# Optimization experiments

Hardware: AMD Instinct MI355X
Metric: run time of the kernel (lower is better)

## Reference

```python
import jax, jax.numpy as jnp
import numpy as np

N = 100000
E = 1600000
IN, HID, OUT = 128, 256, 47


def _glorot(key, shape):
    fan_in, fan_out = shape
    lim = np.sqrt(6.0 / (fan_in + fan_out))
    return jax.random.uniform(key, shape, jnp.float32, -lim, lim)


def setup_inputs() -> dict:
    key = jax.random.key(0)
    ks = jax.random.split(key, 12)
    x = jax.random.normal(ks[0], (N, IN), jnp.float32)
    src = jax.random.randint(ks[1], (E,), 0, N, jnp.int32)
    dst = jax.random.randint(ks[2], (E,), 0, N, jnp.int32)
    dims = [(IN, HID), (HID, HID), (HID, OUT)]
    inp = {"x": x, "src": src, "dst": dst}
    for i, (di, do) in enumerate(dims, 1):
        inp[f"w_self{i}"] = _glorot(ks[2 + 3 * i - 2], (di, do))
        inp[f"w_neigh{i}"] = _glorot(ks[2 + 3 * i - 1], (di, do))
        inp[f"b{i}"] = jnp.zeros((do,), jnp.float32)
    return inp


def sage_conv(x, src, dst, w_self, w_neigh, b):
    n = x.shape[0]
    msg = x[src]                                              # [E, d] gather
    summed = jax.ops.segment_sum(msg, dst, num_segments=n)    # [N, d]
    deg = jax.ops.segment_sum(jnp.ones((src.shape[0],), x.dtype), dst, num_segments=n)
    h_neigh = summed / jnp.maximum(deg, 1.0)[:, None]         # mean aggregate
    return x @ w_self + h_neigh @ w_neigh + b


def reference(x, src, dst, w_self1, w_neigh1, b1, w_self2, w_neigh2, b2, w_self3, w_neigh3, b3):
    h = sage_conv(x, src, dst, w_self1, w_neigh1, b1)
    h = jax.nn.relu(h)  # dropout = identity in eval mode
    h = sage_conv(h, src, dst, w_self2, w_neigh2, b2)
    h = jax.nn.relu(h)
    h = sage_conv(h, src, dst, w_self3, w_neigh3, b3)
    return h
```

## Files before the change

kernel.cpp:

```cpp
#include <hip/hip_runtime.h>

#define N_NODES 100000
#define N_EDGES 1600000

typedef __attribute__((ext_vector_type(8))) _Float16 half8;
typedef __attribute__((ext_vector_type(4))) _Float16 half4v;
typedef __attribute__((ext_vector_type(4))) float floatx4;


__global__ void deg_rank(const int* __restrict__ dst, int* __restrict__ deg,
                         int* __restrict__ rank, int e) {
    int i = blockIdx.x * blockDim.x + threadIdx.x;
    if (i < e) rank[i] = atomicAdd(&deg[dst[i]], 1);
}

__global__ __launch_bounds__(256) void scan_partial(const int* __restrict__ deg,
                                                    int* __restrict__ bsum, int n) {
    __shared__ int wsum[4];
    int t = threadIdx.x;
    int base = blockIdx.x * 2048 + t * 8;
    int tsum = 0;
    #pragma unroll
    for (int k = 0; k < 8; ++k) {
        int idx = base + k;
        tsum += (idx < n) ? deg[idx] : 0;
    }
    #pragma unroll
    for (int d = 1; d < 64; d <<= 1) tsum += __shfl_xor(tsum, d, 64);
    if ((t & 63) == 0) wsum[t >> 6] = tsum;
    __syncthreads();
    if (t == 0) bsum[blockIdx.x] = wsum[0] + wsum[1] + wsum[2] + wsum[3];
}

__global__ void scan_blocksums(const int* __restrict__ bsum, int* __restrict__ bbase, int nb) {
    int t = threadIdx.x;
    int v = (t < nb) ? bsum[t] : 0;
    int s = v;
    #pragma unroll
    for (int d = 1; d < 64; d <<= 1) {
        int u = __shfl_up(s, d, 64);
        if (t >= d) s += u;
    }
    if (t < nb) bbase[t] = s - v;
    if (t == 63) bbase[nb] = s;
}

__global__ __launch_bounds__(256) void scan_write(const int* __restrict__ deg,
                                                  const int* __restrict__ bbase,
                                                  int* __restrict__ offs, int n, int nb) {
    __shared__ int wsum[4];
    int t = threadIdx.x;
    int lane = t & 63, w = t >> 6;
    int base = blockIdx.x * 2048 + t * 8;
    int v[8];
    #pragma unroll
    for (int k = 0; k < 8; ++k) {
        int idx = base + k;
        v[k] = (idx < n) ? deg[idx] : 0;
    }
    int tsum = 0;
    #pragma unroll
    for (int k = 0; k < 8; ++k) { int x = v[k]; v[k] = tsum; tsum += x; }
    int s = tsum;
    #pragma unroll
    for (int d = 1; d < 64; d <<= 1) {
        int u = __shfl_up(s, d, 64);
        if (lane >= d) s += u;
    }
    if (lane == 63) wsum[w] = s;
    __syncthreads();
    int wb = 0;
    for (int j = 0; j < w; ++j) wb += wsum[j];
    int texcl = bbase[blockIdx.x] + wb + (s - tsum);
    #pragma unroll
    for (int k = 0; k < 8; ++k) {
        int idx = base + k;
        if (idx < n) offs[idx] = texcl + v[k];
    }
    if (blockIdx.x == 0 && t == 0) offs[n] = bbase[nb];
}

__global__ void fill_csr2(const int* __restrict__ src, const int* __restrict__ dst,
                          const int* __restrict__ offs, const int* __restrict__ rank,
                          int* __restrict__ csr, int e) {
    int i = blockIdx.x * blockDim.x + threadIdx.x;
    if (i < e) csr[offs[dst[i]] + rank[i]] = src[i];
}


__global__ void cvt_f16(const float4* __restrict__ in, half4v* __restrict__ oh, int n4) {
    int i = blockIdx.x * blockDim.x + threadIdx.x;
    if (i >= n4) return;
    float4 v = in[i];
    half4v h;
    h[0] = (_Float16)v.x; h[1] = (_Float16)v.y;
    h[2] = (_Float16)v.z; h[3] = (_Float16)v.w;
    oh[i] = h;
}


__global__ void prep_all(const float* __restrict__ ws1, const float* __restrict__ wn1,
                         const float* __restrict__ ws2, const float* __restrict__ wn2,
                         const float* __restrict__ ws3, const float* __restrict__ wn3,
                         _Float16* __restrict__ o1s, _Float16* __restrict__ o1n,
                         _Float16* __restrict__ o2s, _Float16* __restrict__ o2n,
                         _Float16* __restrict__ o3c) {
    int i = blockIdx.x * blockDim.x + threadIdx.x;
    if (i < 65536) {
        const float* W = (i < 32768) ? ws1 : wn1;
        _Float16* O = (i < 32768) ? o1s : o1n;
        int j = i & 32767;
        int nn = j >> 7, k = j & 127;
        O[j] = (_Float16)W[k * 256 + nn];
    } else if (i < 196608) {
        int j = i - 65536;
        const float* W = (j < 65536) ? ws2 : wn2;
        _Float16* O = (j < 65536) ? o2s : o2n;
        j &= 65535;
        int nn = j >> 8, k = j & 255;
        O[j] = (_Float16)W[k * 256 + nn];
    } else if (i < 221184) {
        int j = i - 196608;
        const float* W = (j < 12288) ? ws3 : wn3;
        _Float16* O = o3c + ((j < 12288) ? 0 : 12288);
        j = (j < 12288) ? j : j - 12288;
        int nn = j >> 8, k = j & 255;
        O[j] = (nn < 47) ? (_Float16)W[k * 47 + nn] : (_Float16)0.f;
    }
}


__global__ __launch_bounds__(256) void aggP(const _Float16* __restrict__ Xp,
                                            const int* __restrict__ csr,
                                            const int* __restrict__ offs,
                                            _Float16* __restrict__ Pp, int n) {
    int node = blockIdx.x * 4 + (threadIdx.x >> 6);
    int lane = threadIdx.x & 63;
    int qtr = lane >> 4;
    int sl = lane & 15;
    if (node >= n) return;
    int e0 = offs[node], e1 = offs[node + 1];
    float a[8] = {0.f, 0.f, 0.f, 0.f, 0.f, 0.f, 0.f, 0.f};
    int e = e0;
    for (; e + 16 <= e1; e += 16) {
        int s0 = csr[e + qtr];
        int s1 = csr[e + 4 + qtr];
        int s2 = csr[e + 8 + qtr];
        int s3 = csr[e + 12 + qtr];
        half8 u0 = ((const half8*)(Xp + (size_t)s0 * 128))[sl];
        half8 u1 = ((const half8*)(Xp + (size_t)s1 * 128))[sl];
        half8 u2 = ((const half8*)(Xp + (size_t)s2 * 128))[sl];
        half8 u3 = ((const half8*)(Xp + (size_t)s3 * 128))[sl];
        #pragma unroll
        for (int j = 0; j < 8; ++j) a[j] += (float)u0[j];
        #pragma unroll
        for (int j = 0; j < 8; ++j) a[j] += (float)u1[j];
        #pragma unroll
        for (int j = 0; j < 8; ++j) a[j] += (float)u2[j];
        #pragma unroll
        for (int j = 0; j < 8; ++j) a[j] += (float)u3[j];
    }
    for (; e + 8 <= e1; e += 8) {
        int s0 = csr[e + qtr];
        int s1 = csr[e + 4 + qtr];
        half8 u0 = ((const half8*)(Xp + (size_t)s0 * 128))[sl];
        half8 u1 = ((const half8*)(Xp + (size_t)s1 * 128))[sl];
        #pragma unroll
        for (int j = 0; j < 8; ++j) a[j] += (float)u0[j];
        #pragma unroll
        for (int j = 0; j < 8; ++j) a[j] += (float)u1[j];
    }
    for (; e + 4 <= e1; e += 4) {
        int s = csr[e + qtr];
        half8 u = ((const half8*)(Xp + (size_t)s * 128))[sl];
        #pragma unroll
        for (int j = 0; j < 8; ++j) a[j] += (float)u[j];
    }
    int rem = e1 - e;
    if (qtr < rem) {
        int s = csr[e + qtr];
        half8 u = ((const half8*)(Xp + (size_t)s * 128))[sl];
        #pragma unroll
        for (int j = 0; j < 8; ++j) a[j] += (float)u[j];
    }
    #pragma unroll
    for (int j = 0; j < 8; ++j) {
        a[j] += __shfl_xor(a[j], 16);
        a[j] += __shfl_xor(a[j], 32);
    }
    if (lane < 16) {
        float inv = 1.0f / fmaxf((float)(e1 - e0), 1.0f);
        half8 rh;
        #pragma unroll
        for (int j = 0; j < 8; ++j) rh[j] = (_Float16)(a[j] * inv);
        ((half8*)(Pp + (size_t)node * 128))[sl] = rh;
    }
}

__global__ __launch_bounds__(256) void agg_l3(const _Float16* __restrict__ Y,
                                              const float* __restrict__ S,
                                              const int* __restrict__ csr,
                                              const int* __restrict__ offs,
                                              float* __restrict__ out, int n) {
    int node = blockIdx.x * 4 + (threadIdx.x >> 6);
    int lane = threadIdx.x & 63;
    int qtr = lane >> 4;
    int sl = lane & 15;
    int c = sl < 12 ? sl : 11;
    if (node >= n) return;
    int e0 = offs[node], e1 = offs[node + 1];
    float a0 = 0.f, a1 = 0.f, a2 = 0.f, a3 = 0.f;
    int e = e0;
    for (; e + 8 <= e1; e += 8) {
        int s0 = csr[e + qtr];
        int s1 = csr[e + 4 + qtr];
        half4v f0 = ((const half4v*)(Y + (size_t)s0 * 48))[c];
        half4v f1 = ((const half4v*)(Y + (size_t)s1 * 48))[c];
        a0 += (float)f0[0] + (float)f1[0];
        a1 += (float)f0[1] + (float)f1[1];
        a2 += (float)f0[2] + (float)f1[2];
        a3 += (float)f0[3] + (float)f1[3];
    }
    for (; e + 4 <= e1; e += 4) {
        int s = csr[e + qtr];
        half4v f = ((const half4v*)(Y + (size_t)s * 48))[c];
        a0 += (float)f[0]; a1 += (float)f[1]; a2 += (float)f[2]; a3 += (float)f[3];
    }
    int rem = e1 - e;
    if (qtr < rem) {
        int s = csr[e + qtr];
        half4v f = ((const half4v*)(Y + (size_t)s * 48))[c];
        a0 += (float)f[0]; a1 += (float)f[1]; a2 += (float)f[2]; a3 += (float)f[3];
    }
    a0 += __shfl_xor(a0, 16); a0 += __shfl_xor(a0, 32);
    a1 += __shfl_xor(a1, 16); a1 += __shfl_xor(a1, 32);
    a2 += __shfl_xor(a2, 16); a2 += __shfl_xor(a2, 32);
    a3 += __shfl_xor(a3, 16); a3 += __shfl_xor(a3, 32);
    if (lane < 12) {
        float inv = 1.0f / fmaxf((float)(e1 - e0), 1.0f);
        float4 sv = ((const float4*)(S + (size_t)node * 48))[c];
        float r[4] = {sv.x + a0 * inv, sv.y + a1 * inv, sv.z + a2 * inv, sv.w + a3 * inv};
        #pragma unroll
        for (int k = 0; k < 4; ++k) {
            int col = c * 4 + k;
            if (col < 47) out[(size_t)node * 47 + col] = r[k];
        }
    }
}


template <int NTILES, int OUTFMT, int SPP, int PHASES>
__global__ __launch_bounds__(256, 3) void gemm64r(
    const _Float16* __restrict__ A1h, const _Float16* __restrict__ A2h,
    const _Float16* __restrict__ W1, const _Float16* __restrict__ W2,
    const float* __restrict__ bias, float* __restrict__ outS, _Float16* __restrict__ outY,
    _Float16* __restrict__ outh, int n, int relu) {
    constexpr int NPAD = NTILES * 16;
    constexpr int LDT = 36;
    constexpr int NSTEPS = SPP * PHASES;
    constexpr int K = SPP * 32;
    __shared__ _Float16 Bs[2][NPAD * LDT];

    const int t = threadIdx.x;
    const int bm = blockIdx.x * 64;
    const int colbase = blockIdx.y * NPAD;
    const int lane = t & 63;
    const int w = t >> 6;
    const int quad = lane >> 4;
    const int tl = lane & 15;
    const int r0 = bm + w * 16 + tl;
    const size_t PS = (size_t)n * 128;

    floatx4 acc[NTILES];
    #pragma unroll
    for (int j = 0; j < NTILES; ++j) acc[j] = (floatx4){0.f, 0.f, 0.f, 0.f};

    half8 areg[NSTEPS];
    #pragma unroll
    for (int ph = 0; ph < PHASES; ++ph) {
        const _Float16* Ah = (ph == 0) ? A1h : A2h;
        #pragma unroll
        for (int st = 0; st < SPP; ++st) {
            int kq = st * 32 + quad * 8;
            const _Float16* Ab = Ah + ((kq >> 7) ? PS : (size_t)0) + (kq & 127);
            half8 d = (half8){0};
            if (r0 < n) d = *(const half8*)(Ab + (size_t)r0 * 128);
            areg[ph * SPP + st] = d;
        }
    }

    half8 pb0, pb1, pb2, pb3;
    auto wload = [&](int s2) {
        int ph2 = (s2 >= SPP) ? 1 : 0;
        int k02 = (ph2 ? s2 - SPP : s2) * 32;
        const _Float16* W = ph2 ? W2 : W1;
        const half8* p = (const half8*)(W + (size_t)(colbase + t) * K + k02);
        pb0 = p[0]; pb1 = p[1]; pb2 = p[2]; pb3 = p[3];
    };

    if (t < NPAD) {
        wload(0);
        *(half8*)&Bs[0][t * LDT + 0]  = pb0;
        *(half8*)&Bs[0][t * LDT + 8]  = pb1;
        *(half8*)&Bs[0][t * LDT + 16] = pb2;
        *(half8*)&Bs[0][t * LDT + 24] = pb3;
        if (NSTEPS > 1) wload(1);
    }
    __syncthreads();

    #pragma unroll
    for (int s = 0; s < NSTEPS; ++s) {
        const int cur = s & 1;
        if (s + 1 < NSTEPS && t < NPAD) {
            *(half8*)&Bs[cur ^ 1][t * LDT + 0]  = pb0;
            *(half8*)&Bs[cur ^ 1][t * LDT + 8]  = pb1;
            *(half8*)&Bs[cur ^ 1][t * LDT + 16] = pb2;
            *(half8*)&Bs[cur ^ 1][t * LDT + 24] = pb3;
            if (s + 2 < NSTEPS) wload(s + 2);
        }
        half8 ca = areg[s];
        #pragma unroll
        for (int nt = 0; nt < NTILES; ++nt) {
            half8 bh = *(const half8*)&Bs[cur][(nt * 16 + tl) * LDT + quad * 8];
            acc[nt] = __builtin_amdgcn_mfma_f32_16x16x32_f16(ca, bh, acc[nt], 0, 0, 0);
        }
        asm volatile("s_waitcnt lgkmcnt(0)" ::: "memory");
        __builtin_amdgcn_sched_barrier(0);
        __builtin_amdgcn_s_barrier();
    }

    #pragma unroll
    for (int nt = 0; nt < NTILES; ++nt) {
        int gc = colbase + nt * 16 + tl;
        #pragma unroll
        for (int r = 0; r < 4; ++r) {
            int gr = bm + w * 16 + quad * 4 + r;
            if (gr >= n) continue;
            float v = acc[nt][r];
            if (OUTFMT == 1) {
                v += bias[gc];
                if (relu) v = fmaxf(v, 0.f);
                outh[(size_t)(gc >> 7) * PS + (size_t)gr * 128 + (gc & 127)] = (_Float16)v;
            } else {
                if (gc < 48) {
                    v += (gc < 47) ? bias[gc] : 0.f;
                    outS[(size_t)gr * 48 + gc] = v;
                } else {
                    outY[(size_t)gr * 48 + (gc - 48)] = (_Float16)v;
                }
            }
        }
    }
}


template <int NTILES, int OUTFMT>
__global__ __launch_bounds__(256, 2) void gemm_mfma(
    const _Float16* __restrict__ A1h, const _Float16* __restrict__ A2h,
    const _Float16* __restrict__ W1, const _Float16* __restrict__ W2,
    const float* __restrict__ bias, float* __restrict__ outS, _Float16* __restrict__ outY,
    _Float16* __restrict__ outh, int n, int K, int dout, int relu, int phases) {
    constexpr int NPAD = NTILES * 16;
    constexpr int LDT = 36;
    __shared__ _Float16 Bs[2][NPAD * LDT];

    const int t = threadIdx.x;
    const int bm = blockIdx.x * 128;
    const int lane = t & 63;
    const int w = t >> 6;
    const int quad = lane >> 4;
    const int tl = lane & 15;
    const int r0 = bm + w * 32 + tl;
    const int r1 = r0 + 16;
    const size_t PS = (size_t)n * 128;

    floatx4 acc[2][NTILES];
    #pragma unroll
    for (int i = 0; i < 2; ++i)
        #pragma unroll
        for (int j = 0; j < NTILES; ++j) acc[i][j] = (floatx4){0.f, 0.f, 0.f, 0.f};

    const int spp = K >> 5;
    const int nsteps = phases * spp;

    half8 pb0, pb1, pb2, pb3;
    half8 a0A = {0}, a1A = {0}, a0B = {0}, a1B = {0};

    auto wload = [&](int s2) {
        int ph2 = (s2 >= spp) ? 1 : 0;
        int k02 = (ph2 ? s2 - spp : s2) << 5;
        const _Float16* W = ph2 ? W2 : W1;
        const half8* p = (const half8*)(W + (size_t)t * K + k02);
        pb0 = p[0]; pb1 = p[1]; pb2 = p[2]; pb3 = p[3];
    };
    auto aload = [&](int s2, half8& d0, half8& d1) {
        int ph2 = (s2 >= spp) ? 1 : 0;
        int k02 = (ph2 ? s2 - spp : s2) << 5;
        const _Float16* Ah = ph2 ? A2h : A1h;
        int kq = k02 + quad * 8;
        const _Float16* Ab = Ah + ((kq >> 7) ? PS : (size_t)0) + (kq & 127);
        d0 = (half8){0}; d1 = (half8){0};
        if (r0 < n) d0 = *(const half8*)(Ab + (size_t)r0 * 128);
        if (r1 < n) d1 = *(const half8*)(Ab + (size_t)r1 * 128);
    };

    if (t < NPAD) {
        wload(0);
        *(half8*)&Bs[0][t * LDT + 0]  = pb0;
        *(half8*)&Bs[0][t * LDT + 8]  = pb1;
        *(half8*)&Bs[0][t * LDT + 16] = pb2;
        *(half8*)&Bs[0][t * LDT + 24] = pb3;
        wload(1);
    }
    aload(0, a0A, a1A);
    aload(1, a0B, a1B);
    __syncthreads();

    for (int s = 0; s < nsteps; s += 2) {
        {
            if (s + 1 < nsteps && t < NPAD) {
                *(half8*)&Bs[1][t * LDT + 0]  = pb0;
                *(half8*)&Bs[1][t * LDT + 8]  = pb1;
                *(half8*)&Bs[1][t * LDT + 16] = pb2;
                *(half8*)&Bs[1][t * LDT + 24] = pb3;
                if (s + 2 < nsteps) wload(s + 2);
            }
            half8 ca0 = a0A, ca1 = a1A;
            if (s + 2 < nsteps) aload(s + 2, a0A, a1A);
            #pragma unroll
            for (int nt = 0; nt < NTILES; ++nt) {
                half8 bh = *(const half8*)&Bs[0][(nt * 16 + tl) * LDT + quad * 8];
                acc[0][nt] = __builtin_amdgcn_mfma_f32_16x16x32_f16(ca0, bh, acc[0][nt], 0, 0, 0);
                acc[1][nt] = __builtin_amdgcn_mfma_f32_16x16x32_f16(ca1, bh, acc[1][nt], 0, 0, 0);
            }
            asm volatile("s_waitcnt lgkmcnt(0)" ::: "memory");
            __builtin_amdgcn_sched_barrier(0);
            __builtin_amdgcn_s_barrier();
        }
        {
            int s1 = s + 1;
            if (s1 + 1 < nsteps && t < NPAD) {
                *(half8*)&Bs[0][t * LDT + 0]  = pb0;
                *(half8*)&Bs[0][t * LDT + 8]  = pb1;
                *(half8*)&Bs[0][t * LDT + 16] = pb2;
                *(half8*)&Bs[0][t * LDT + 24] = pb3;
                if (s1 + 2 < nsteps) wload(s1 + 2);
            }
            half8 ca0 = a0B, ca1 = a1B;
            if (s1 + 2 < nsteps) aload(s1 + 2, a0B, a1B);
            #pragma unroll
            for (int nt = 0; nt < NTILES; ++nt) {
                half8 bh = *(const half8*)&Bs[1][(nt * 16 + tl) * LDT + quad * 8];
                acc[0][nt] = __builtin_amdgcn_mfma_f32_16x16x32_f16(ca0, bh, acc[0][nt], 0, 0, 0);
                acc[1][nt] = __builtin_amdgcn_mfma_f32_16x16x32_f16(ca1, bh, acc[1][nt], 0, 0, 0);
            }
            asm volatile("s_waitcnt lgkmcnt(0)" ::: "memory");
            __builtin_amdgcn_sched_barrier(0);
            __builtin_amdgcn_s_barrier();
        }
    }

    #pragma unroll
    for (int mt = 0; mt < 2; ++mt) {
        #pragma unroll
        for (int nt = 0; nt < NTILES; ++nt) {
            int gc = nt * 16 + tl;
            if (OUTFMT == 1 && gc >= dout) continue;
            #pragma unroll
            for (int r = 0; r < 4; ++r) {
                int gr = bm + w * 32 + mt * 16 + quad * 4 + r;
                if (gr >= n) continue;
                float v = acc[mt][nt][r];
                if (OUTFMT == 1) {
                    v += bias[gc];
                    if (relu) v = fmaxf(v, 0.f);
                    outh[(size_t)(gc >> 7) * PS + (size_t)gr * 128 + (gc & 127)] = (_Float16)v;
                } else {
                    if (gc < 48) {
                        v += (gc < 47) ? bias[gc] : 0.f;
                        outS[(size_t)gr * 48 + gc] = v;
                    } else {
                        outY[(size_t)gr * 48 + (gc - 48)] = (_Float16)v;
                    }
                }
            }
        }
    }
}

extern "C" void kernel_launch(void* const* d_in, const int* in_sizes, int n_in,
                              void* d_out, int out_size, void* d_ws, size_t ws_size,
                              hipStream_t stream) {
    (void)in_sizes; (void)n_in; (void)out_size;
    const int N = N_NODES, E = N_EDGES;
    const float* x = (const float*)d_in[0];
    const int* src = (const int*)d_in[1];
    const int* dst = (const int*)d_in[2];
    const float* w_self1 = (const float*)d_in[3];
    const float* w_neigh1 = (const float*)d_in[4];
    const float* b1 = (const float*)d_in[5];
    const float* w_self2 = (const float*)d_in[6];
    const float* w_neigh2 = (const float*)d_in[7];
    const float* b2 = (const float*)d_in[8];
    const float* w_self3 = (const float*)d_in[9];
    const float* w_neigh3 = (const float*)d_in[10];
    const float* b3 = (const float*)d_in[11];
    float* out = (float*)d_out;

    _Float16* Ph = (_Float16*)d_ws;
    _Float16* Hh = Ph + (size_t)N * 256;
    int* deg = (int*)(Hh + (size_t)N * 256);
    int* offs = deg + N;
    int* csr = offs + N + 4;
    _Float16* wbuf = (_Float16*)(csr + E);
    _Float16* w1s = wbuf;
    _Float16* w1n = w1s + 32768;
    _Float16* w2s = w1n + 32768;
    _Float16* w2n = w2s + 65536;
    _Float16* w3c = w2n + 65536;
    int* bsum = (int*)(w3c + 24576);
    int* bbase = bsum + 64;
    int* rank = (int*)Ph;
    _Float16* xh = Ph + (size_t)N * 128;
    float* S = (float*)Ph;
    _Float16* Y = (_Float16*)(S + (size_t)N * 48);
    size_t used = (size_t)((char*)(bbase + 64) - (char*)d_ws);
    used = (used + 255) & ~(size_t)255;
    _Float16* H2 = (_Float16*)((char*)d_ws + used);
    const bool dbuf = (used + (size_t)N * 256 * sizeof(_Float16)) <= ws_size;

    const int NB = (N + 2047) / 2048;

    hipMemsetAsync(deg, 0, N * sizeof(int), stream);
    deg_rank<<<(E + 255) / 256, 256, 0, stream>>>(dst, deg, rank, E);
    scan_partial<<<NB, 256, 0, stream>>>(deg, bsum, N);
    scan_blocksums<<<1, 64, 0, stream>>>(bsum, bbase, NB);
    scan_write<<<NB, 256, 0, stream>>>(deg, bbase, offs, N, NB);
    fill_csr2<<<(E + 255) / 256, 256, 0, stream>>>(src, dst, offs, rank, csr, E);

    cvt_f16<<<(N * 128 / 4 + 255) / 256, 256, 0, stream>>>((const float4*)x, (half4v*)xh,
                                                           N * 128 / 4);
    prep_all<<<(221184 + 255) / 256, 256, 0, stream>>>(w_self1, w_neigh1, w_self2, w_neigh2,
                                                       w_self3, w_neigh3, w1s, w1n, w2s, w2n,
                                                       w3c);

    const int g64 = (N + 63) / 64;
    int aggGrid = (N + 3) / 4;

    aggP<<<aggGrid, 256, 0, stream>>>(xh, csr, offs, Ph, N);
    gemm64r<8, 1, 4, 2><<<dim3(g64, 2), 256, 0, stream>>>(xh, Ph, w1s, w1n, b1, nullptr,
                                                          nullptr, Hh, N, 1);
    aggP<<<aggGrid, 256, 0, stream>>>(Hh, csr, offs, Ph, N);
    aggP<<<aggGrid, 256, 0, stream>>>(Hh + (size_t)N * 128, csr, offs, Ph + (size_t)N * 128, N);
    const _Float16* Hcur;
    if (dbuf) {
        gemm64r<8, 1, 8, 2><<<dim3(g64, 2), 256, 0, stream>>>(Hh, Ph, w2s, w2n, b2, nullptr,
                                                              nullptr, H2, N, 1);
        Hcur = H2;
    } else {
        gemm_mfma<16, 1><<<(N + 127) / 128, 256, 0, stream>>>(Hh, Ph, w2s, w2n, b2, nullptr,
                                                              nullptr, Hh, N, 256, 256, 1, 2);
        Hcur = Hh;
    }
    gemm64r<6, 2, 8, 1><<<dim3(g64, 1), 256, 0, stream>>>(Hcur, nullptr, w3c, nullptr, b3,
                                                          S, Y, nullptr, N, 0);
    agg_l3<<<aggGrid, 256, 0, stream>>>(Y, S, csr, offs, out, N);
}
```

Measured before the change: 636.4 us.

## Keep weight tiles in registers and loop over row tiles per block

Replaces the LDS double-buffered weight staging GEMM with a kernel where each wave holds its weight columns in registers for the whole K dimension and walks eight 16-row tiles, double-buffering A loads in registers. This removes LDS writes, barriers and repeated weight loads per 64-row block, and amortises the weight fetch over 128 rows. In exchange register pressure rises sharply (for layer 2 about 32 half8 B registers per lane), which may lower occupancy. Layer 3 now wastes a wave's worth of columns (96 of 128), clamped by ncols.

```diff
diff --git a/kernel.cpp b/kernel.cpp
--- a/kernel.cpp
+++ b/kernel.cpp
@@ -249,107 +249,100 @@
 }
 
 
-template <int NTILES, int OUTFMT, int SPP, int PHASES>
-__global__ __launch_bounds__(256, 3) void gemm64r(
+template <int NTPW, int OUTFMT, int SPP, int PHASES, int MT>
+__global__ __launch_bounds__(256) void gemm_breg(
     const _Float16* __restrict__ A1h, const _Float16* __restrict__ A2h,
     const _Float16* __restrict__ W1, const _Float16* __restrict__ W2,
-    const float* __restrict__ bias, float* __restrict__ outS, _Float16* __restrict__ outY,
-    _Float16* __restrict__ outh, int n, int relu) {
-    constexpr int NPAD = NTILES * 16;
-    constexpr int LDT = 36;
+    const float* __restrict__ bias, float* __restrict__ outS,
+    _Float16* __restrict__ outY, _Float16* __restrict__ outh,
+    int n, int relu, int ncols) {
     constexpr int NSTEPS = SPP * PHASES;
     constexpr int K = SPP * 32;
-    __shared__ _Float16 Bs[2][NPAD * LDT];
-
     const int t = threadIdx.x;
-    const int bm = blockIdx.x * 64;
-    const int colbase = blockIdx.y * NPAD;
     const int lane = t & 63;
     const int w = t >> 6;
     const int quad = lane >> 4;
     const int tl = lane & 15;
-    const int r0 = bm + w * 16 + tl;
+    const int colw = blockIdx.y * 128 + w * (NTPW * 16);
     const size_t PS = (size_t)n * 128;
 
-    floatx4 acc[NTILES];
-    #pragma unroll
-    for (int j = 0; j < NTILES; ++j) acc[j] = (floatx4){0.f, 0.f, 0.f, 0.f};
-
-    half8 areg[NSTEPS];
-    #pragma unroll
-    for (int ph = 0; ph < PHASES; ++ph) {
-        const _Float16* Ah = (ph == 0) ? A1h : A2h;
-        #pragma unroll
-        for (int st = 0; st < SPP; ++st) {
-            int kq = st * 32 + quad * 8;
-            const _Float16* Ab = Ah + ((kq >> 7) ? PS : (size_t)0) + (kq & 127);
-            half8 d = (half8){0};
-            if (r0 < n) d = *(const half8*)(Ab + (size_t)r0 * 128);
-            areg[ph * SPP + st] = d;
-        }
-    }
-
-    half8 pb0, pb1, pb2, pb3;
-    auto wload = [&](int s2) {
-        int ph2 = (s2 >= SPP) ? 1 : 0;
-        int k02 = (ph2 ? s2 - SPP : s2) * 32;
-        const _Float16* W = ph2 ? W2 : W1;
-        const half8* p = (const half8*)(W + (size_t)(colbase + t) * K + k02);
-        pb0 = p[0]; pb1 = p[1]; pb2 = p[2]; pb3 = p[3];
+    half8 breg[NTPW][NSTEPS];
+    #pragma unroll
+    for (int nt = 0; nt < NTPW; ++nt) {
+        int col = colw + nt * 16 + tl;
+        int colc = (col < ncols) ? col : (ncols - 1);
+        #pragma unroll
+        for (int ph = 0; ph < PHASES; ++ph) {
+            const _Float16* W = (ph == 0) ? W1 : W2;
+            const half8* p = (const half8*)(W + (size_t)colc * K + quad * 8);
+            #pragma unroll
+            for (int st = 0; st < SPP; ++st)
+                breg[nt][ph * SPP + st] = p[st * 4];
+        }
+    }
+
+    auto loadA = [&](int rowbase, half8 (&a)[NSTEPS]) {
+        int r0 = rowbase + tl;
+        #pragma unroll
+        for (int ph = 0; ph < PHASES; ++ph) {
+            const _Float16* Ah = (ph == 0) ? A1h : A2h;
+            #pragma unroll
+            for (int st = 0; st < SPP; ++st) {
+                int kq = st * 32 + quad * 8;
+                const _Float16* Ab = Ah + ((kq >> 7) ? PS : (size_t)0) + (kq & 127);
+                half8 d = (half8){0};
+                if (r0 < n) d = *(const half8*)(Ab + (size_t)r0 * 128);
+                a[ph * SPP + st] = d;
+            }
+        }
     };
 
-    if (t < NPAD) {
-        wload(0);
-        *(half8*)&Bs[0][t * LDT + 0]  = pb0;
-        *(half8*)&Bs[0][t * LDT + 8]  = pb1;
-        *(half8*)&Bs[0][t * LDT + 16] = pb2;
-        *(half8*)&Bs[0][t * LDT + 24] = pb3;
-        if (NSTEPS > 1) wload(1);
-    }
-    __syncthreads();
-
-    #pragma unroll
-    for (int s = 0; s < NSTEPS; ++s) {
-        const int cur = s & 1;
-        if (s + 1 < NSTEPS && t < NPAD) {
-            *(half8*)&Bs[cur ^ 1][t * LDT + 0]  = pb0;
-            *(half8*)&Bs[cur ^ 1][t * LDT + 8]  = pb1;
-            *(half8*)&Bs[cur ^ 1][t * LDT + 16] = pb2;
-            *(half8*)&Bs[cur ^ 1][t * LDT + 24] = pb3;
-            if (s + 2 < NSTEPS) wload(s + 2);
-        }
-        half8 ca = areg[s];
-        #pragma unroll
-        for (int nt = 0; nt < NTILES; ++nt) {
-            half8 bh = *(const half8*)&Bs[cur][(nt * 16 + tl) * LDT + quad * 8];
-            acc[nt] = __builtin_amdgcn_mfma_f32_16x16x32_f16(ca, bh, acc[nt], 0, 0, 0);
-        }
-        asm volatile("s_waitcnt lgkmcnt(0)" ::: "memory");
-        __builtin_amdgcn_sched_barrier(0);
-        __builtin_amdgcn_s_barrier();
-    }
-
-    #pragma unroll
-    for (int nt = 0; nt < NTILES; ++nt) {
-        int gc = colbase + nt * 16 + tl;
-        #pragma unroll
-        for (int r = 0; r < 4; ++r) {
-            int gr = bm + w * 16 + quad * 4 + r;
-            if (gr >= n) continue;
-            float v = acc[nt][r];
-            if (OUTFMT == 1) {
-                v += bias[gc];
-                if (relu) v = fmaxf(v, 0.f);
-                outh[(size_t)(gc >> 7) * PS + (size_t)gr * 128 + (gc & 127)] = (_Float16)v;
-            } else {
-                if (gc < 48) {
-                    v += (gc < 47) ? bias[gc] : 0.f;
-                    outS[(size_t)gr * 48 + gc] = v;
+    auto compute_store = [&](int rowbase, half8 (&a)[NSTEPS]) {
+        floatx4 acc[NTPW];
+        #pragma unroll
+        for (int nt = 0; nt < NTPW; ++nt) acc[nt] = (floatx4){0.f, 0.f, 0.f, 0.f};
+        #pragma unroll
+        for (int s = 0; s < NSTEPS; ++s) {
+            #pragma unroll
+            for (int nt = 0; nt < NTPW; ++nt)
+                acc[nt] = __builtin_amdgcn_mfma_f32_16x16x32_f16(a[s], breg[nt][s],
+                                                                 acc[nt], 0, 0, 0);
+        }
+        #pragma unroll
+        for (int nt = 0; nt < NTPW; ++nt) {
+            int gc = colw + nt * 16 + tl;
+            if (gc >= ncols) continue;
+            #pragma unroll
+            for (int r = 0; r < 4; ++r) {
+                int gr = rowbase + quad * 4 + r;
+                if (gr >= n) continue;
+                float v = acc[nt][r];
+                if (OUTFMT == 1) {
+                    v += bias[gc];
+                    if (relu) v = fmaxf(v, 0.f);
+                    outh[(size_t)(gc >> 7) * PS + (size_t)gr * 128 + (gc & 127)] = (_Float16)v;
                 } else {
-                    outY[(size_t)gr * 48 + (gc - 48)] = (_Float16)v;
+                    if (gc < 48) {
+                        v += (gc < 47) ? bias[gc] : 0.f;
+                        outS[(size_t)gr * 48 + gc] = v;
+                    } else {
+                        outY[(size_t)gr * 48 + (gc - 48)] = (_Float16)v;
+                    }
                 }
             }
         }
+    };
+
+    int rowbase = blockIdx.x * (MT * 16);
+    half8 aA[NSTEPS], aB[NSTEPS];
+    loadA(rowbase, aA);
+    #pragma unroll
+    for (int m = 0; m < MT; m += 2) {
+        if (m + 1 < MT) loadA(rowbase + 16, aB);
+        compute_store(rowbase, aA);
+        if (m + 2 < MT) loadA(rowbase + 32, aA);
+        if (m + 1 < MT) compute_store(rowbase + 16, aB);
+        rowbase += 32;
     }
 }
 
@@ -544,25 +537,26 @@
                                                        w_self3, w_neigh3, w1s, w1n, w2s, w2n,
                                                        w3c);
 
-    const int g64 = (N + 63) / 64;
+    const int gB = (N + 127) / 128;
     int aggGrid = (N + 3) / 4;
 
     aggP<<<aggGrid, 256, 0, stream>>>(xh, csr, offs, Ph, N);
-    gemm64r<8, 1, 4, 2><<<dim3(g64, 2), 256, 0, stream>>>(xh, Ph, w1s, w1n, b1, nullptr,
-                                                          nullptr, Hh, N, 1);
+    gemm_breg<2, 1, 4, 2, 8><<<dim3(gB, 2), 256, 0, stream>>>(xh, Ph, w1s, w1n, b1, nullptr,
+                                                              nullptr, Hh, N, 1, 256);
     aggP<<<aggGrid, 256, 0, stream>>>(Hh, csr, offs, Ph, N);
     aggP<<<aggGrid, 256, 0, stream>>>(Hh + (size_t)N * 128, csr, offs, Ph + (size_t)N * 128, N);
     const _Float16* Hcur;
     if (dbuf) {
-        gemm64r<8, 1, 8, 2><<<dim3(g64, 2), 256, 0, stream>>>(Hh, Ph, w2s, w2n, b2, nullptr,
-                                                              nullptr, H2, N, 1);
+        gemm_breg<2, 1, 8, 2, 8><<<dim3(gB, 2), 256, 0, stream>>>(Hh, Ph, w2s, w2n, b2,
+                                                                  nullptr, nullptr, H2, N, 1,
+                                                                  256);
         Hcur = H2;
     } else {
         gemm_mfma<16, 1><<<(N + 127) / 128, 256, 0, stream>>>(Hh, Ph, w2s, w2n, b2, nullptr,
                                                               nullptr, Hh, N, 256, 256, 1, 2);
         Hcur = Hh;
     }
-    gemm64r<6, 2, 8, 1><<<dim3(g64, 1), 256, 0, stream>>>(Hcur, nullptr, w3c, nullptr, b3,
-                                                          S, Y, nullptr, N, 0);
+    gemm_breg<2, 2, 8, 1, 8><<<dim3(gB, 1), 256, 0, stream>>>(Hcur, nullptr, w3c, nullptr,
+                                                              b3, S, Y, nullptr, N, 0, 96);
     agg_l3<<<aggGrid, 256, 0, stream>>>(Y, S, csr, offs, out, N);
 }
```

Measured after the change: 814.0 us. 1.28x slower.
